# Performance work log

Hardware: AMD Instinct MI355X
Metric: run time of the kernel (lower is better)

The kernel has to match this reference:

```python
import jax, jax.numpy as jnp
import numpy as np

N = 50000      # nodes
E = 800000     # edges (avg degree 16)
F = 128        # num_features
H = 128        # hidden_channels
C = 16         # num_classes
KEEP = 0.5     # dropout keep prob


def setup_inputs() -> dict:
    key = jax.random.key(0)
    ks = jax.random.split(key, 7)
    x = jax.random.normal(ks[0], (N, F), dtype=jnp.float32)
    edge_index = jax.random.randint(ks[1], (2, E), 0, N, dtype=jnp.int64)
    W1 = jax.random.normal(ks[2], (F, H), dtype=jnp.float32) / np.float32(np.sqrt(F))
    b1 = jnp.zeros((H,), dtype=jnp.float32)
    W2 = jax.random.normal(ks[3], (H, C), dtype=jnp.float32) / np.float32(np.sqrt(H))
    b2 = jnp.zeros((C,), dtype=jnp.float32)
    # deterministic dropout mask (train-mode dropout, prob=0.5), pre-scaled by 1/keep
    dropout_mask = (jax.random.uniform(ks[4], (N, H)) < KEEP).astype(jnp.float32) / np.float32(KEEP)
    return {"x": x, "edge_index": edge_index, "W1": W1, "b1": b1,
            "W2": W2, "b2": b2, "dropout_mask": dropout_mask}


def _gather_mean(h, src, dst, n_nodes):
    # irregular gather (h[src]) + segment scatter-add at dst, then mean by in-degree
    agg = jax.ops.segment_sum(h[src], dst, num_segments=n_nodes)  # [N, c]
    deg = jax.ops.segment_sum(jnp.ones_like(dst, dtype=h.dtype), dst, num_segments=n_nodes)
    return agg / jnp.maximum(deg, 1.0)[:, None]


def reference(x, edge_index, W1, b1, W2, b2, dropout_mask):
    src, dst = edge_index[0], edge_index[1]
    # linmaps1: 0th->1st order broadcast; identity for singleton reference domains
    h = _gather_mean(x, src, dst, N)          # ConvolutionalLayer_1P #1: gather
    h = h @ W1 + b1                           # linear transform
    h = jax.nn.relu(h)
    h = h * dropout_mask                      # Dropout(prob=0.5)
    h = _gather_mean(h, src, dst, N)          # ConvolutionalLayer_1P #2: gather
    out = h @ W2 + b2
    # linmaps0: 1st->0th order reduce; identity for singleton domains
    return out
```

## Files before the change

kernel.cpp:

```cpp
#include <hip/hip_runtime.h>

#define NNODES 50000
#define NEDGES 800000
#define FDIM 128
#define HDIM 128
#define CDIM 16

#define NBUCK 256
#define BCAP 6144
#define NBA 391
#define NMB 782

typedef __attribute__((ext_vector_type(8))) short bf16x8;
typedef __attribute__((ext_vector_type(4))) float f32x4;

__device__ __forceinline__ ushort f32_to_bf16_rne(float f) {
  unsigned u = __float_as_uint(f);
  unsigned rounded = u + 0x7fffu + ((u >> 16) & 1u);
  return (ushort)(rounded >> 16);
}
__device__ __forceinline__ float bf_lo(unsigned u) { return __uint_as_float(u << 16); }
__device__ __forceinline__ float bf_hi(unsigned u) { return __uint_as_float(u & 0xffff0000u); }

__global__ __launch_bounds__(256) void k_binA(
    const int* __restrict__ src, const int* __restrict__ dst,
    int* __restrict__ gcur, unsigned* __restrict__ ebuf,
    const float* __restrict__ mask, unsigned* __restrict__ maskb) {
  __shared__ int cnt[NBUCK];
  __shared__ int base[NBUCK];
  int tid = threadIdx.x;
  if (blockIdx.x < NBA) {
    int e0 = blockIdx.x * 2048;
    cnt[tid] = 0;
    __syncthreads();
    int sv[8], dv[8];
    #pragma unroll
    for (int i = 0; i < 8; ++i) {
      int e = e0 + i * 256 + tid;
      if (e < NEDGES) {
        sv[i] = src[e];
        dv[i] = dst[e];
        atomicAdd(&cnt[dv[i] >> 8], 1);
      } else {
        dv[i] = -1;
      }
    }
    __syncthreads();
    base[tid] = atomicAdd(&gcur[tid], cnt[tid]);
    cnt[tid] = 0;
    __syncthreads();
    #pragma unroll
    for (int i = 0; i < 8; ++i) {
      if (dv[i] >= 0) {
        int b = dv[i] >> 8;
        int pos = base[b] + atomicAdd(&cnt[b], 1);
        if (pos < BCAP)
          ebuf[b * BCAP + pos] = ((unsigned)(dv[i] & 255) << 16) | (unsigned)sv[i];
      }
    }
    return;
  }
  int t = (blockIdx.x - NBA) * 256 + tid;
  if (t < 200000) {
    const float* mp = mask + (size_t)t * 32;
    unsigned bits = 0;
    #pragma unroll
    for (int i = 0; i < 8; ++i) {
      float4 m = *reinterpret_cast<const float4*>(mp + i * 4);
      bits |= (m.x != 0.f ? 1u : 0u) << (i * 4 + 0);
      bits |= (m.y != 0.f ? 1u : 0u) << (i * 4 + 1);
      bits |= (m.z != 0.f ? 1u : 0u) << (i * 4 + 2);
      bits |= (m.w != 0.f ? 1u : 0u) << (i * 4 + 3);
    }
    maskb[t] = bits;
  }
}

__global__ __launch_bounds__(256) void k_binB_cast(
    const int* __restrict__ gcur, const unsigned* __restrict__ ebuf,
    int* __restrict__ deg, int* __restrict__ offs, ushort* __restrict__ ssrc,
    const float* __restrict__ x, ushort* __restrict__ xh,
    const float* __restrict__ W1, ushort* __restrict__ W1T,
    const float* __restrict__ W2, ushort* __restrict__ W2T) {
  __shared__ int s[NBUCK];
  __shared__ int doff[NBUCK];
  __shared__ int dcur[NBUCK];
  int tid = threadIdx.x;
  if (blockIdx.x < NBUCK) {
    int b = blockIdx.x;
    int c = gcur[tid];
    if (c > BCAP) c = BCAP;
    s[tid] = c;
    for (int off = 1; off < 256; off <<= 1) {
      __syncthreads();
      int t = (tid >= off) ? s[tid - off] : 0;
      __syncthreads();
      s[tid] += t;
    }
    __syncthreads();
    int my_base = (b > 0) ? s[b - 1] : 0;
    int count = s[b] - my_base;

    dcur[tid] = 0;
    __syncthreads();
    const unsigned* eb = &ebuf[b * BCAP];
    for (int e = tid; e < count; e += 256) {
      atomicAdd(&dcur[eb[e] >> 16], 1);
    }
    __syncthreads();
    int dn = dcur[tid];
    s[tid] = dn;
    for (int off = 1; off < 256; off <<= 1) {
      __syncthreads();
      int t = (tid >= off) ? s[tid - off] : 0;
      __syncthreads();
      s[tid] += t;
    }
    __syncthreads();
    doff[tid] = s[tid] - dn;
    int node = b * 256 + tid;
    if (node < NNODES) {
      deg[node] = dn;
      offs[node] = my_base + doff[tid];
    }
    dcur[tid] = 0;
    __syncthreads();

    for (int e = tid; e < count; e += 256) {
      unsigned v = eb[e];
      int loc = v >> 16;
      int pos = my_base + doff[loc] + atomicAdd(&dcur[loc], 1);
      ssrc[pos] = (ushort)(v & 0xffffu);
    }
    return;
  }
  int t = (blockIdx.x - NBUCK) * 256 + tid;
  if (t < 1600000) {
    float4 v = *reinterpret_cast<const float4*>(&x[t * 4]);
    ushort4 o;
    o.x = f32_to_bf16_rne(v.x);
    o.y = f32_to_bf16_rne(v.y);
    o.z = f32_to_bf16_rne(v.z);
    o.w = f32_to_bf16_rne(v.w);
    *reinterpret_cast<ushort4*>(&xh[t * 4]) = o;
    return;
  }
  t -= 1600000;
  if (t < 16384) {
    int c = t >> 7, k = t & 127;
    W1T[c * 128 + k] = f32_to_bf16_rne(W1[k * 128 + c]);
    return;
  }
  t -= 16384;
  if (t < 2048) {
    int c = t >> 7, k = t & 127;
    W2T[c * 128 + k] = f32_to_bf16_rne(W2[k * 16 + c]);
  }
}

#define ACCA(A, U) do { \
    A[0] += bf_lo(U.x); A[1] += bf_hi(U.x); \
    A[2] += bf_lo(U.y); A[3] += bf_hi(U.y); \
    A[4] += bf_lo(U.z); A[5] += bf_hi(U.z); \
    A[6] += bf_lo(U.w); A[7] += bf_hi(U.w); } while (0)

#define HT_STRIDE 132
__global__ __launch_bounds__(256) void k_fused1(
    const ushort* __restrict__ xh, const int* __restrict__ offs,
    const int* __restrict__ deg, const ushort* __restrict__ ssrc,
    const ushort* __restrict__ W1T, const float* __restrict__ b1,
    const unsigned* __restrict__ maskb, const ushort* __restrict__ W2T,
    ushort* __restrict__ zh) {
  __shared__ ushort sh[16 * HT_STRIDE];
  __shared__ ushort ht[16 * HT_STRIDE];
  int tid = threadIdx.x;
  int grp = tid >> 4;
  int l16 = tid & 15;
  int nw = blockIdx.x * 16;
  int n = nw + grp;
  int start = offs[n];
  int d = deg[n];
  const ushort* base = xh + l16 * 8;
  float a0[8] = {0,0,0,0,0,0,0,0};
  float a1[8] = {0,0,0,0,0,0,0,0};
  float a2[8] = {0,0,0,0,0,0,0,0};
  float a3[8] = {0,0,0,0,0,0,0,0};
  int j = 0;
  for (; j + 7 < d; j += 8) {
    int s0 = ssrc[start + j + 0];
    int s1 = ssrc[start + j + 1];
    int s2 = ssrc[start + j + 2];
    int s3 = ssrc[start + j + 3];
    int s4 = ssrc[start + j + 4];
    int s5 = ssrc[start + j + 5];
    int s6 = ssrc[start + j + 6];
    int s7 = ssrc[start + j + 7];
    uint4 u0 = *reinterpret_cast<const uint4*>(base + s0 * FDIM);
    uint4 u1 = *reinterpret_cast<const uint4*>(base + s1 * FDIM);
    uint4 u2 = *reinterpret_cast<const uint4*>(base + s2 * FDIM);
    uint4 u3 = *reinterpret_cast<const uint4*>(base + s3 * FDIM);
    uint4 u4 = *reinterpret_cast<const uint4*>(base + s4 * FDIM);
    uint4 u5 = *reinterpret_cast<const uint4*>(base + s5 * FDIM);
    uint4 u6 = *reinterpret_cast<const uint4*>(base + s6 * FDIM);
    uint4 u7 = *reinterpret_cast<const uint4*>(base + s7 * FDIM);
    ACCA(a0, u0); ACCA(a1, u1); ACCA(a2, u2); ACCA(a3, u3);
    ACCA(a0, u4); ACCA(a1, u5); ACCA(a2, u6); ACCA(a3, u7);
  }
  for (; j + 3 < d; j += 4) {
    int s0 = ssrc[start + j + 0];
    int s1 = ssrc[start + j + 1];
    int s2 = ssrc[start + j + 2];
    int s3 = ssrc[start + j + 3];
    uint4 u0 = *reinterpret_cast<const uint4*>(base + s0 * FDIM);
    uint4 u1 = *reinterpret_cast<const uint4*>(base + s1 * FDIM);
    uint4 u2 = *reinterpret_cast<const uint4*>(base + s2 * FDIM);
    uint4 u3 = *reinterpret_cast<const uint4*>(base + s3 * FDIM);
    ACCA(a0, u0); ACCA(a1, u1); ACCA(a2, u2); ACCA(a3, u3);
  }
  for (; j < d; ++j) {
    int s0 = ssrc[start + j];
    uint4 u0 = *reinterpret_cast<const uint4*>(base + s0 * FDIM);
    ACCA(a0, u0);
  }
  float inv = 1.0f / (float)(d > 0 ? d : 1);
  unsigned r[4];
  #pragma unroll
  for (int k = 0; k < 4; ++k) {
    float e0 = (a0[2 * k] + a1[2 * k] + a2[2 * k] + a3[2 * k]) * inv;
    float e1 = (a0[2 * k + 1] + a1[2 * k + 1] + a2[2 * k + 1] + a3[2 * k + 1]) * inv;
    r[k] = (unsigned)f32_to_bf16_rne(e0) | ((unsigned)f32_to_bf16_rne(e1) << 16);
  }
  *reinterpret_cast<uint4*>(&sh[grp * HT_STRIDE + l16 * 8]) =
      (uint4){r[0], r[1], r[2], r[3]};
  __syncthreads();

  int w = tid >> 6;
  int lane = tid & 63;
  int m = lane & 15, quad = lane >> 4;
  int ct0 = 2 * w, ct1 = 2 * w + 1;

  bf16x8 af[4];
  #pragma unroll
  for (int kk = 0; kk < 4; ++kk) {
    const ushort* ap = &sh[m * HT_STRIDE + kk * 32 + quad * 8];
    ushort4 alo = *reinterpret_cast<const ushort4*>(ap);
    ushort4 ahi = *reinterpret_cast<const ushort4*>(ap + 4);
    af[kk] = (bf16x8){(short)alo.x, (short)alo.y, (short)alo.z, (short)alo.w,
                      (short)ahi.x, (short)ahi.y, (short)ahi.z, (short)ahi.w};
  }
  f32x4 acc0 = (f32x4){0.f, 0.f, 0.f, 0.f};
  f32x4 acc1 = (f32x4){0.f, 0.f, 0.f, 0.f};
  const ushort* bp0 = &W1T[(size_t)(ct0 * 16 + m) * 128 + quad * 8];
  const ushort* bp1 = &W1T[(size_t)(ct1 * 16 + m) * 128 + quad * 8];
  #pragma unroll
  for (int kk = 0; kk < 4; ++kk) {
    acc0 = __builtin_amdgcn_mfma_f32_16x16x32_bf16(
        af[kk], *reinterpret_cast<const bf16x8*>(bp0 + kk * 32), acc0, 0, 0, 0);
    acc1 = __builtin_amdgcn_mfma_f32_16x16x32_bf16(
        af[kk], *reinterpret_cast<const bf16x8*>(bp1 + kk * 32), acc1, 0, 0, 0);
  }

  unsigned mbw[4];
  #pragma unroll
  for (int rr = 0; rr < 4; ++rr) {
    mbw[rr] = maskb[(size_t)(nw + quad * 4 + rr) * 4 + w];
  }
  float bb0 = b1[ct0 * 16 + m];
  float bb1 = b1[ct1 * 16 + m];
  int sh0 = m;
  int sh1 = 16 + m;
  #pragma unroll
  for (int rr = 0; rr < 4; ++rr) {
    float v0 = acc0[rr] + bb0;
    v0 = v0 > 0.f ? v0 : 0.f;
    v0 = ((mbw[rr] >> sh0) & 1u) ? (v0 + v0) : 0.f;
    ht[(quad * 4 + rr) * HT_STRIDE + ct0 * 16 + m] = f32_to_bf16_rne(v0);
    float v1 = acc1[rr] + bb1;
    v1 = v1 > 0.f ? v1 : 0.f;
    v1 = ((mbw[rr] >> sh1) & 1u) ? (v1 + v1) : 0.f;
    ht[(quad * 4 + rr) * HT_STRIDE + ct1 * 16 + m] = f32_to_bf16_rne(v1);
  }
  __syncthreads();

  if (w == 0) {
    f32x4 zacc = (f32x4){0.f, 0.f, 0.f, 0.f};
    #pragma unroll
    for (int kk = 0; kk < 4; ++kk) {
      const ushort* ap = &ht[m * HT_STRIDE + kk * 32 + quad * 8];
      ushort4 alo = *reinterpret_cast<const ushort4*>(ap);
      ushort4 ahi = *reinterpret_cast<const ushort4*>(ap + 4);
      bf16x8 afr = (bf16x8){(short)alo.x, (short)alo.y, (short)alo.z, (short)alo.w,
                            (short)ahi.x, (short)ahi.y, (short)ahi.z, (short)ahi.w};
      bf16x8 b2f = *reinterpret_cast<const bf16x8*>(&W2T[m * 128 + kk * 32 + quad * 8]);
      zacc = __builtin_amdgcn_mfma_f32_16x16x32_bf16(afr, b2f, zacc, 0, 0, 0);
    }
    #pragma unroll
    for (int rr = 0; rr < 4; ++rr) {
      zh[(size_t)(nw + quad * 4 + rr) * 16 + m] = f32_to_bf16_rne(zacc[rr]);
    }
  }
}

__global__ __launch_bounds__(256) void k_spmm2(
    const ushort* __restrict__ zh, const int* __restrict__ offs,
    const int* __restrict__ deg, const ushort* __restrict__ ssrc,
    const float* __restrict__ b2, float* __restrict__ out) {
  int tid = threadIdx.x;
  int nl = tid >> 3, c2 = tid & 7;
  int n = blockIdx.x * 32 + nl;
  if (n >= NNODES) return;
  int start = offs[n], d = deg[n];
  const ushort* zb = zh + c2 * 2;
  float a0 = 0.f, a1 = 0.f, b0 = 0.f, b1v = 0.f;
  float c0 = 0.f, c1 = 0.f, d0 = 0.f, d1 = 0.f;
  int j = 0;
  for (; j + 7 < d; j += 8) {
    int s0 = ssrc[start + j + 0], s1 = ssrc[start + j + 1];
    int s2 = ssrc[start + j + 2], s3 = ssrc[start + j + 3];
    int s4 = ssrc[start + j + 4], s5 = ssrc[start + j + 5];
    int s6 = ssrc[start + j + 6], s7 = ssrc[start + j + 7];
    unsigned u0 = *reinterpret_cast<const unsigned*>(zb + s0 * 16);
    unsigned u1 = *reinterpret_cast<const unsigned*>(zb + s1 * 16);
    unsigned u2 = *reinterpret_cast<const unsigned*>(zb + s2 * 16);
    unsigned u3 = *reinterpret_cast<const unsigned*>(zb + s3 * 16);
    unsigned u4 = *reinterpret_cast<const unsigned*>(zb + s4 * 16);
    unsigned u5 = *reinterpret_cast<const unsigned*>(zb + s5 * 16);
    unsigned u6 = *reinterpret_cast<const unsigned*>(zb + s6 * 16);
    unsigned u7 = *reinterpret_cast<const unsigned*>(zb + s7 * 16);
    a0 += bf_lo(u0); a1 += bf_hi(u0);
    b0 += bf_lo(u1); b1v += bf_hi(u1);
    c0 += bf_lo(u2); c1 += bf_hi(u2);
    d0 += bf_lo(u3); d1 += bf_hi(u3);
    a0 += bf_lo(u4); a1 += bf_hi(u4);
    b0 += bf_lo(u5); b1v += bf_hi(u5);
    c0 += bf_lo(u6); c1 += bf_hi(u6);
    d0 += bf_lo(u7); d1 += bf_hi(u7);
  }
  for (; j < d; ++j) {
    int s0 = ssrc[start + j];
    unsigned u0 = *reinterpret_cast<const unsigned*>(zb + s0 * 16);
    a0 += bf_lo(u0); a1 += bf_hi(u0);
  }
  float inv = 1.0f / (float)(d > 0 ? d : 1);
  float o0 = ((a0 + b0) + (c0 + d0)) * inv + b2[c2 * 2 + 0];
  float o1 = ((a1 + b1v) + (c1 + d1)) * inv + b2[c2 * 2 + 1];
  float2 o; o.x = o0; o.y = o1;
  *reinterpret_cast<float2*>(&out[(size_t)n * 16 + c2 * 2]) = o;
}


extern "C" void kernel_launch(void* const* d_in, const int* in_sizes, int n_in,
                              void* d_out, int out_size, void* d_ws, size_t ws_size,
                              hipStream_t stream) {
  const float* x    = (const float*)d_in[0];
  const int*   ei   = (const int*)d_in[1];
  const float* W1   = (const float*)d_in[2];
  const float* b1   = (const float*)d_in[3];
  const float* W2   = (const float*)d_in[4];
  const float* b2   = (const float*)d_in[5];
  const float* mask = (const float*)d_in[6];
  float* out = (float*)d_out;

  const int* src = ei;
  const int* dst = ei + NEDGES;

  char* ws = (char*)d_ws;
  size_t o = 0;
  auto alloc = [&](size_t bytes) -> void* {
    void* p = ws + o;
    o += (bytes + 255) & ~(size_t)255;
    return p;
  };
  ushort*   xh    = (ushort*)alloc((size_t)NNODES * 128 * 2);
  ushort*   zh    = (ushort*)alloc((size_t)NNODES * 16 * 2);
  ushort*   W1T   = (ushort*)alloc((size_t)128 * 128 * 2);
  ushort*   W2T   = (ushort*)alloc((size_t)16 * 128 * 2);
  int*      deg   = (int*)alloc((size_t)NNODES * 4);
  int*      offs  = (int*)alloc((size_t)NNODES * 4);
  int*      gcur  = (int*)alloc((size_t)NBUCK * 4);
  unsigned* ebuf  = (unsigned*)alloc((size_t)NBUCK * BCAP * 4);
  ushort*   ssrc  = (ushort*)alloc((size_t)NEDGES * 2);
  unsigned* maskb = (unsigned*)alloc((size_t)NNODES * 4 * 4);

  int cast_blocks = (1600000 + 16384 + 2048 + 255) / 256;

  hipMemsetAsync(gcur, 0, NBUCK * sizeof(int), stream);
  k_binA<<<NBA + NMB, 256, 0, stream>>>(src, dst, gcur, ebuf, mask, maskb);
  k_binB_cast<<<NBUCK + cast_blocks, 256, 0, stream>>>(gcur, ebuf, deg, offs, ssrc,
                                                       x, xh, W1, W1T, W2, W2T);
  k_fused1<<<NNODES / 16, 256, 0, stream>>>(xh, offs, deg, ssrc,
                                            W1T, b1, maskb, W2T, zh);
  k_spmm2<<<(NNODES + 31) / 32, 256, 0, stream>>>(zh, offs, deg, ssrc, b2, out);
}
```

Before: 173.5 us.

## Merge four-kernel pipeline into one persistent cooperative kernel with grid syncs

Result: slower. 624.8 us (+260.2%).

```diff
diff --git a/kernel.cpp b/kernel.cpp
--- a/kernel.cpp
+++ b/kernel.cpp
@@ -1,15 +1,21 @@
 #include <hip/hip_runtime.h>
+#include <hip/hip_cooperative_groups.h>
+
+namespace cg = cooperative_groups;
 
 #define NNODES 50000
 #define NEDGES 800000
 #define FDIM 128
-#define HDIM 128
-#define CDIM 16
 
 #define NBUCK 256
 #define BCAP 6144
 #define NBA 391
 #define NMB 782
+#define CASTU 6322
+#define A_UNITS (NBA + NMB + CASTU)
+#define C_TILES 3125
+#define D_UNITS 1563
+#define HT_STRIDE 132
 
 typedef __attribute__((ext_vector_type(8))) short bf16x8;
 typedef __attribute__((ext_vector_type(4))) float f32x4;
@@ -22,72 +28,113 @@
 __device__ __forceinline__ float bf_lo(unsigned u) { return __uint_as_float(u << 16); }
 __device__ __forceinline__ float bf_hi(unsigned u) { return __uint_as_float(u & 0xffff0000u); }
 
-__global__ __launch_bounds__(256) void k_binA(
+#define ACCA(A, U) do { \
+    A[0] += bf_lo(U.x); A[1] += bf_hi(U.x); \
+    A[2] += bf_lo(U.y); A[3] += bf_hi(U.y); \
+    A[4] += bf_lo(U.z); A[5] += bf_hi(U.z); \
+    A[6] += bf_lo(U.w); A[7] += bf_hi(U.w); } while (0)
+
+__global__ __launch_bounds__(256, 8) void k_mega(
     const int* __restrict__ src, const int* __restrict__ dst,
-    int* __restrict__ gcur, unsigned* __restrict__ ebuf,
-    const float* __restrict__ mask, unsigned* __restrict__ maskb) {
-  __shared__ int cnt[NBUCK];
-  __shared__ int base[NBUCK];
+    const float* __restrict__ x, const float* __restrict__ W1,
+    const float* __restrict__ b1, const float* __restrict__ W2,
+    const float* __restrict__ b2, const float* __restrict__ mask,
+    float* __restrict__ out,
+    ushort* __restrict__ xh, ushort* __restrict__ zh,
+    ushort* __restrict__ W1T, ushort* __restrict__ W2T,
+    int* __restrict__ deg, int* __restrict__ offs, int* __restrict__ gcur,
+    unsigned* __restrict__ ebuf, ushort* __restrict__ ssrc,
+    unsigned* __restrict__ maskb) {
+  cg::grid_group grid = cg::this_grid();
+  __shared__ __align__(16) char smem[8448];
+  int* si = (int*)smem;
+  ushort* su = (ushort*)smem;
   int tid = threadIdx.x;
-  if (blockIdx.x < NBA) {
-    int e0 = blockIdx.x * 2048;
-    cnt[tid] = 0;
-    __syncthreads();
-    int sv[8], dv[8];
-    #pragma unroll
-    for (int i = 0; i < 8; ++i) {
-      int e = e0 + i * 256 + tid;
-      if (e < NEDGES) {
-        sv[i] = src[e];
-        dv[i] = dst[e];
-        atomicAdd(&cnt[dv[i] >> 8], 1);
+  int G = gridDim.x;
+
+  if (blockIdx.x == 0) gcur[tid] = 0;
+  grid.sync();
+
+  for (int u = blockIdx.x; u < A_UNITS; u += G) {
+    if (u < NBA) {
+      int* cnt = si;
+      int* base = si + NBUCK;
+      int e0 = u * 2048;
+      cnt[tid] = 0;
+      __syncthreads();
+      int sv[8], dv[8];
+      #pragma unroll
+      for (int i = 0; i < 8; ++i) {
+        int e = e0 + i * 256 + tid;
+        if (e < NEDGES) {
+          sv[i] = src[e];
+          dv[i] = dst[e];
+          atomicAdd(&cnt[dv[i] >> 8], 1);
+        } else {
+          dv[i] = -1;
+        }
+      }
+      __syncthreads();
+      base[tid] = atomicAdd(&gcur[tid], cnt[tid]);
+      cnt[tid] = 0;
+      __syncthreads();
+      #pragma unroll
+      for (int i = 0; i < 8; ++i) {
+        if (dv[i] >= 0) {
+          int b = dv[i] >> 8;
+          int pos = base[b] + atomicAdd(&cnt[b], 1);
+          if (pos < BCAP)
+            ebuf[b * BCAP + pos] = ((unsigned)(dv[i] & 255) << 16) | (unsigned)sv[i];
+        }
+      }
+      __syncthreads();
+    } else if (u < NBA + NMB) {
+      int t = (u - NBA) * 256 + tid;
+      if (t < 200000) {
+        const float* mp = mask + (size_t)t * 32;
+        unsigned bits = 0;
+        #pragma unroll
+        for (int i = 0; i < 8; ++i) {
+          float4 m = *reinterpret_cast<const float4*>(mp + i * 4);
+          bits |= (m.x != 0.f ? 1u : 0u) << (i * 4 + 0);
+          bits |= (m.y != 0.f ? 1u : 0u) << (i * 4 + 1);
+          bits |= (m.z != 0.f ? 1u : 0u) << (i * 4 + 2);
+          bits |= (m.w != 0.f ? 1u : 0u) << (i * 4 + 3);
+        }
+        maskb[t] = bits;
+      }
+    } else {
+      int t = (u - NBA - NMB) * 256 + tid;
+      if (t < 1600000) {
+        float4 v = *reinterpret_cast<const float4*>(&x[t * 4]);
+        ushort4 o;
+        o.x = f32_to_bf16_rne(v.x);
+        o.y = f32_to_bf16_rne(v.y);
+        o.z = f32_to_bf16_rne(v.z);
+        o.w = f32_to_bf16_rne(v.w);
+        *reinterpret_cast<ushort4*>(&xh[t * 4]) = o;
       } else {
-        dv[i] = -1;
-      }
-    }
-    __syncthreads();
-    base[tid] = atomicAdd(&gcur[tid], cnt[tid]);
-    cnt[tid] = 0;
-    __syncthreads();
-    #pragma unroll
-    for (int i = 0; i < 8; ++i) {
-      if (dv[i] >= 0) {
-        int b = dv[i] >> 8;
-        int pos = base[b] + atomicAdd(&cnt[b], 1);
-        if (pos < BCAP)
-          ebuf[b * BCAP + pos] = ((unsigned)(dv[i] & 255) << 16) | (unsigned)sv[i];
-      }
-    }
-    return;
+        t -= 1600000;
+        if (t < 16384) {
+          int c = t >> 7, k = t & 127;
+          W1T[c * 128 + k] = f32_to_bf16_rne(W1[k * 128 + c]);
+        } else {
+          t -= 16384;
+          if (t < 2048) {
+            int c = t >> 7, k = t & 127;
+            W2T[c * 128 + k] = f32_to_bf16_rne(W2[k * 16 + c]);
+          }
+        }
+      }
+    }
   }
-  int t = (blockIdx.x - NBA) * 256 + tid;
-  if (t < 200000) {
-    const float* mp = mask + (size_t)t * 32;
-    unsigned bits = 0;
-    #pragma unroll
-    for (int i = 0; i < 8; ++i) {
-      float4 m = *reinterpret_cast<const float4*>(mp + i * 4);
-      bits |= (m.x != 0.f ? 1u : 0u) << (i * 4 + 0);
-      bits |= (m.y != 0.f ? 1u : 0u) << (i * 4 + 1);
-      bits |= (m.z != 0.f ? 1u : 0u) << (i * 4 + 2);
-      bits |= (m.w != 0.f ? 1u : 0u) << (i * 4 + 3);
-    }
-    maskb[t] = bits;
-  }
-}
-
-__global__ __launch_bounds__(256) void k_binB_cast(
-    const int* __restrict__ gcur, const unsigned* __restrict__ ebuf,
-    int* __restrict__ deg, int* __restrict__ offs, ushort* __restrict__ ssrc,
-    const float* __restrict__ x, ushort* __restrict__ xh,
-    const float* __restrict__ W1, ushort* __restrict__ W1T,
-    const float* __restrict__ W2, ushort* __restrict__ W2T) {
-  __shared__ int s[NBUCK];
-  __shared__ int doff[NBUCK];
-  __shared__ int dcur[NBUCK];
-  int tid = threadIdx.x;
-  if (blockIdx.x < NBUCK) {
-    int b = blockIdx.x;
+  grid.sync();
+
+  for (int u = blockIdx.x; u < NBUCK; u += G) {
+    int* s = si;
+    int* doff = si + NBUCK;
+    int* dcur = si + 2 * NBUCK;
+    int b = u;
     int c = gcur[tid];
     if (c > BCAP) c = BCAP;
     s[tid] = c;
@@ -132,220 +179,176 @@
       int pos = my_base + doff[loc] + atomicAdd(&dcur[loc], 1);
       ssrc[pos] = (ushort)(v & 0xffffu);
     }
-    return;
+    __syncthreads();
   }
-  int t = (blockIdx.x - NBUCK) * 256 + tid;
-  if (t < 1600000) {
-    float4 v = *reinterpret_cast<const float4*>(&x[t * 4]);
-    ushort4 o;
-    o.x = f32_to_bf16_rne(v.x);
-    o.y = f32_to_bf16_rne(v.y);
-    o.z = f32_to_bf16_rne(v.z);
-    o.w = f32_to_bf16_rne(v.w);
-    *reinterpret_cast<ushort4*>(&xh[t * 4]) = o;
-    return;
-  }
-  t -= 1600000;
-  if (t < 16384) {
-    int c = t >> 7, k = t & 127;
-    W1T[c * 128 + k] = f32_to_bf16_rne(W1[k * 128 + c]);
-    return;
-  }
-  t -= 16384;
-  if (t < 2048) {
-    int c = t >> 7, k = t & 127;
-    W2T[c * 128 + k] = f32_to_bf16_rne(W2[k * 16 + c]);
-  }
-}
-
-#define ACCA(A, U) do { \
-    A[0] += bf_lo(U.x); A[1] += bf_hi(U.x); \
-    A[2] += bf_lo(U.y); A[3] += bf_hi(U.y); \
-    A[4] += bf_lo(U.z); A[5] += bf_hi(U.z); \
-    A[6] += bf_lo(U.w); A[7] += bf_hi(U.w); } while (0)
-
-#define HT_STRIDE 132
-__global__ __launch_bounds__(256) void k_fused1(
-    const ushort* __restrict__ xh, const int* __restrict__ offs,
-    const int* __restrict__ deg, const ushort* __restrict__ ssrc,
-    const ushort* __restrict__ W1T, const float* __restrict__ b1,
-    const unsigned* __restrict__ maskb, const ushort* __restrict__ W2T,
-    ushort* __restrict__ zh) {
-  __shared__ ushort sh[16 * HT_STRIDE];
-  __shared__ ushort ht[16 * HT_STRIDE];
-  int tid = threadIdx.x;
-  int grp = tid >> 4;
-  int l16 = tid & 15;
-  int nw = blockIdx.x * 16;
-  int n = nw + grp;
-  int start = offs[n];
-  int d = deg[n];
-  const ushort* base = xh + l16 * 8;
-  float a0[8] = {0,0,0,0,0,0,0,0};
-  float a1[8] = {0,0,0,0,0,0,0,0};
-  float a2[8] = {0,0,0,0,0,0,0,0};
-  float a3[8] = {0,0,0,0,0,0,0,0};
-  int j = 0;
-  for (; j + 7 < d; j += 8) {
-    int s0 = ssrc[start + j + 0];
-    int s1 = ssrc[start + j + 1];
-    int s2 = ssrc[start + j + 2];
-    int s3 = ssrc[start + j + 3];
-    int s4 = ssrc[start + j + 4];
-    int s5 = ssrc[start + j + 5];
-    int s6 = ssrc[start + j + 6];
-    int s7 = ssrc[start + j + 7];
-    uint4 u0 = *reinterpret_cast<const uint4*>(base + s0 * FDIM);
-    uint4 u1 = *reinterpret_cast<const uint4*>(base + s1 * FDIM);
-    uint4 u2 = *reinterpret_cast<const uint4*>(base + s2 * FDIM);
-    uint4 u3 = *reinterpret_cast<const uint4*>(base + s3 * FDIM);
-    uint4 u4 = *reinterpret_cast<const uint4*>(base + s4 * FDIM);
-    uint4 u5 = *reinterpret_cast<const uint4*>(base + s5 * FDIM);
-    uint4 u6 = *reinterpret_cast<const uint4*>(base + s6 * FDIM);
-    uint4 u7 = *reinterpret_cast<const uint4*>(base + s7 * FDIM);
-    ACCA(a0, u0); ACCA(a1, u1); ACCA(a2, u2); ACCA(a3, u3);
-    ACCA(a0, u4); ACCA(a1, u5); ACCA(a2, u6); ACCA(a3, u7);
-  }
-  for (; j + 3 < d; j += 4) {
-    int s0 = ssrc[start + j + 0];
-    int s1 = ssrc[start + j + 1];
-    int s2 = ssrc[start + j + 2];
-    int s3 = ssrc[start + j + 3];
-    uint4 u0 = *reinterpret_cast<const uint4*>(base + s0 * FDIM);
-    uint4 u1 = *reinterpret_cast<const uint4*>(base + s1 * FDIM);
-    uint4 u2 = *reinterpret_cast<const uint4*>(base + s2 * FDIM);
-    uint4 u3 = *reinterpret_cast<const uint4*>(base + s3 * FDIM);
-    ACCA(a0, u0); ACCA(a1, u1); ACCA(a2, u2); ACCA(a3, u3);
-  }
-  for (; j < d; ++j) {
-    int s0 = ssrc[start + j];
-    uint4 u0 = *reinterpret_cast<const uint4*>(base + s0 * FDIM);
-    ACCA(a0, u0);
-  }
-  float inv = 1.0f / (float)(d > 0 ? d : 1);
-  unsigned r[4];
-  #pragma unroll
-  for (int k = 0; k < 4; ++k) {
-    float e0 = (a0[2 * k] + a1[2 * k] + a2[2 * k] + a3[2 * k]) * inv;
-    float e1 = (a0[2 * k + 1] + a1[2 * k + 1] + a2[2 * k + 1] + a3[2 * k + 1]) * inv;
-    r[k] = (unsigned)f32_to_bf16_rne(e0) | ((unsigned)f32_to_bf16_rne(e1) << 16);
-  }
-  *reinterpret_cast<uint4*>(&sh[grp * HT_STRIDE + l16 * 8]) =
-      (uint4){r[0], r[1], r[2], r[3]};
-  __syncthreads();
-
-  int w = tid >> 6;
-  int lane = tid & 63;
-  int m = lane & 15, quad = lane >> 4;
-  int ct0 = 2 * w, ct1 = 2 * w + 1;
-
-  bf16x8 af[4];
-  #pragma unroll
-  for (int kk = 0; kk < 4; ++kk) {
-    const ushort* ap = &sh[m * HT_STRIDE + kk * 32 + quad * 8];
-    ushort4 alo = *reinterpret_cast<const ushort4*>(ap);
-    ushort4 ahi = *reinterpret_cast<const ushort4*>(ap + 4);
-    af[kk] = (bf16x8){(short)alo.x, (short)alo.y, (short)alo.z, (short)alo.w,
-                      (short)ahi.x, (short)ahi.y, (short)ahi.z, (short)ahi.w};
-  }
-  f32x4 acc0 = (f32x4){0.f, 0.f, 0.f, 0.f};
-  f32x4 acc1 = (f32x4){0.f, 0.f, 0.f, 0.f};
-  const ushort* bp0 = &W1T[(size_t)(ct0 * 16 + m) * 128 + quad * 8];
-  const ushort* bp1 = &W1T[(size_t)(ct1 * 16 + m) * 128 + quad * 8];
-  #pragma unroll
-  for (int kk = 0; kk < 4; ++kk) {
-    acc0 = __builtin_amdgcn_mfma_f32_16x16x32_bf16(
-        af[kk], *reinterpret_cast<const bf16x8*>(bp0 + kk * 32), acc0, 0, 0, 0);
-    acc1 = __builtin_amdgcn_mfma_f32_16x16x32_bf16(
-        af[kk], *reinterpret_cast<const bf16x8*>(bp1 + kk * 32), acc1, 0, 0, 0);
-  }
-
-  unsigned mbw[4];
-  #pragma unroll
-  for (int rr = 0; rr < 4; ++rr) {
-    mbw[rr] = maskb[(size_t)(nw + quad * 4 + rr) * 4 + w];
-  }
-  float bb0 = b1[ct0 * 16 + m];
-  float bb1 = b1[ct1 * 16 + m];
-  int sh0 = m;
-  int sh1 = 16 + m;
-  #pragma unroll
-  for (int rr = 0; rr < 4; ++rr) {
-    float v0 = acc0[rr] + bb0;
-    v0 = v0 > 0.f ? v0 : 0.f;
-    v0 = ((mbw[rr] >> sh0) & 1u) ? (v0 + v0) : 0.f;
-    ht[(quad * 4 + rr) * HT_STRIDE + ct0 * 16 + m] = f32_to_bf16_rne(v0);
-    float v1 = acc1[rr] + bb1;
-    v1 = v1 > 0.f ? v1 : 0.f;
-    v1 = ((mbw[rr] >> sh1) & 1u) ? (v1 + v1) : 0.f;
-    ht[(quad * 4 + rr) * HT_STRIDE + ct1 * 16 + m] = f32_to_bf16_rne(v1);
-  }
-  __syncthreads();
-
-  if (w == 0) {
-    f32x4 zacc = (f32x4){0.f, 0.f, 0.f, 0.f};
+  grid.sync();
+
+  for (int u = blockIdx.x; u < C_TILES; u += G) {
+    ushort* sh = su;
+    ushort* ht = su + 2112;
+    int grp = tid >> 4;
+    int l16 = tid & 15;
+    int nw = u * 16;
+    int n = nw + grp;
+    int start = offs[n];
+    int d = deg[n];
+    const ushort* base = xh + l16 * 8;
+    float a0[8] = {0,0,0,0,0,0,0,0};
+    float a1[8] = {0,0,0,0,0,0,0,0};
+    float a2[8] = {0,0,0,0,0,0,0,0};
+    float a3[8] = {0,0,0,0,0,0,0,0};
+    int j = 0;
+    for (; j + 3 < d; j += 4) {
+      int s0 = ssrc[start + j + 0];
+      int s1 = ssrc[start + j + 1];
+      int s2 = ssrc[start + j + 2];
+      int s3 = ssrc[start + j + 3];
+      uint4 u0 = *reinterpret_cast<const uint4*>(base + s0 * FDIM);
+      uint4 u1 = *reinterpret_cast<const uint4*>(base + s1 * FDIM);
+      uint4 u2 = *reinterpret_cast<const uint4*>(base + s2 * FDIM);
+      uint4 u3 = *reinterpret_cast<const uint4*>(base + s3 * FDIM);
+      ACCA(a0, u0); ACCA(a1, u1); ACCA(a2, u2); ACCA(a3, u3);
+    }
+    if (j < d) {
+      int s0 = ssrc[start + j];
+      uint4 u0 = *reinterpret_cast<const uint4*>(base + s0 * FDIM);
+      ACCA(a0, u0);
+      ++j;
+      if (j < d) {
+        int s1 = ssrc[start + j];
+        uint4 u1 = *reinterpret_cast<const uint4*>(base + s1 * FDIM);
+        ACCA(a1, u1);
+        ++j;
+        if (j < d) {
+          int s2 = ssrc[start + j];
+          uint4 u2 = *reinterpret_cast<const uint4*>(base + s2 * FDIM);
+          ACCA(a2, u2);
+        }
+      }
+    }
+    float inv = 1.0f / (float)(d > 0 ? d : 1);
+    unsigned r[4];
+    #pragma unroll
+    for (int k = 0; k < 4; ++k) {
+      float e0 = (a0[2 * k] + a1[2 * k] + a2[2 * k] + a3[2 * k]) * inv;
+      float e1 = (a0[2 * k + 1] + a1[2 * k + 1] + a2[2 * k + 1] + a3[2 * k + 1]) * inv;
+      r[k] = (unsigned)f32_to_bf16_rne(e0) | ((unsigned)f32_to_bf16_rne(e1) << 16);
+    }
+    *reinterpret_cast<uint4*>(&sh[grp * HT_STRIDE + l16 * 8]) =
+        (uint4){r[0], r[1], r[2], r[3]};
+    __syncthreads();
+
+    int w = tid >> 6;
+    int lane = tid & 63;
+    int m = lane & 15, quad = lane >> 4;
+    int ct0 = 2 * w, ct1 = 2 * w + 1;
+
+    bf16x8 af[4];
     #pragma unroll
     for (int kk = 0; kk < 4; ++kk) {
-      const ushort* ap = &ht[m * HT_STRIDE + kk * 32 + quad * 8];
+      const ushort* ap = &sh[m * HT_STRIDE + kk * 32 + quad * 8];
       ushort4 alo = *reinterpret_cast<const ushort4*>(ap);
       ushort4 ahi = *reinterpret_cast<const ushort4*>(ap + 4);
-      bf16x8 afr = (bf16x8){(short)alo.x, (short)alo.y, (short)alo.z, (short)alo.w,
-                            (short)ahi.x, (short)ahi.y, (short)ahi.z, (short)ahi.w};
-      bf16x8 b2f = *reinterpret_cast<const bf16x8*>(&W2T[m * 128 + kk * 32 + quad * 8]);
-      zacc = __builtin_amdgcn_mfma_f32_16x16x32_bf16(afr, b2f, zacc, 0, 0, 0);
-    }
+      af[kk] = (bf16x8){(short)alo.x, (short)alo.y, (short)alo.z, (short)alo.w,
+                        (short)ahi.x, (short)ahi.y, (short)ahi.z, (short)ahi.w};
+    }
+    f32x4 acc0 = (f32x4){0.f, 0.f, 0.f, 0.f};
+    f32x4 acc1 = (f32x4){0.f, 0.f, 0.f, 0.f};
+    const ushort* bp0 = &W1T[(size_t)(ct0 * 16 + m) * 128 + quad * 8];
+    const ushort* bp1 = &W1T[(size_t)(ct1 * 16 + m) * 128 + quad * 8];
+    #pragma unroll
+    for (int kk = 0; kk < 4; ++kk) {
+      acc0 = __builtin_amdgcn_mfma_f32_16x16x32_bf16(
+          af[kk], *reinterpret_cast<const bf16x8*>(bp0 + kk * 32), acc0, 0, 0, 0);
+      acc1 = __builtin_amdgcn_mfma_f32_16x16x32_bf16(
+          af[kk], *reinterpret_cast<const bf16x8*>(bp1 + kk * 32), acc1, 0, 0, 0);
+    }
+
+    unsigned mbw[4];
     #pragma unroll
     for (int rr = 0; rr < 4; ++rr) {
-      zh[(size_t)(nw + quad * 4 + rr) * 16 + m] = f32_to_bf16_rne(zacc[rr]);
+      mbw[rr] = maskb[(size_t)(nw + quad * 4 + rr) * 4 + w];
+    }
+    float bb0 = b1[ct0 * 16 + m];
+    float bb1 = b1[ct1 * 16 + m];
+    int sh0 = m;
+    int sh1 = 16 + m;
+    #pragma unroll
+    for (int rr = 0; rr < 4; ++rr) {
+      float v0 = acc0[rr] + bb0;
+      v0 = v0 > 0.f ? v0 : 0.f;
+      v0 = ((mbw[rr] >> sh0) & 1u) ? (v0 + v0) : 0.f;
+      ht[(quad * 4 + rr) * HT_STRIDE + ct0 * 16 + m] = f32_to_bf16_rne(v0);
+      float v1 = acc1[rr] + bb1;
+      v1 = v1 > 0.f ? v1 : 0.f;
+      v1 = ((mbw[rr] >> sh1) & 1u) ? (v1 + v1) : 0.f;
+      ht[(quad * 4 + rr) * HT_STRIDE + ct1 * 16 + m] = f32_to_bf16_rne(v1);
+    }
+    __syncthreads();
+
+    if (w == 0) {
+      f32x4 zacc = (f32x4){0.f, 0.f, 0.f, 0.f};
+      #pragma unroll
+      for (int kk = 0; kk < 4; ++kk) {
+        const ushort* ap = &ht[m * HT_STRIDE + kk * 32 + quad * 8];
+        ushort4 alo = *reinterpret_cast<const ushort4*>(ap);
+        ushort4 ahi = *reinterpret_cast<const ushort4*>(ap + 4);
+        bf16x8 afr = (bf16x8){(short)alo.x, (short)alo.y, (short)alo.z, (short)alo.w,
+                              (short)ahi.x, (short)ahi.y, (short)ahi.z, (short)ahi.w};
+        bf16x8 b2f = *reinterpret_cast<const bf16x8*>(&W2T[m * 128 + kk * 32 + quad * 8]);
+        zacc = __builtin_amdgcn_mfma_f32_16x16x32_bf16(afr, b2f, zacc, 0, 0, 0);
+      }
+      #pragma unroll
+      for (int rr = 0; rr < 4; ++rr) {
+        zh[(size_t)(nw + quad * 4 + rr) * 16 + m] = f32_to_bf16_rne(zacc[rr]);
+      }
     }
   }
-}
-
-__global__ __launch_bounds__(256) void k_spmm2(
-    const ushort* __restrict__ zh, const int* __restrict__ offs,
-    const int* __restrict__ deg, const ushort* __restrict__ ssrc,
-    const float* __restrict__ b2, float* __restrict__ out) {
-  int tid = threadIdx.x;
-  int nl = tid >> 3, c2 = tid & 7;
-  int n = blockIdx.x * 32 + nl;
-  if (n >= NNODES) return;
-  int start = offs[n], d = deg[n];
-  const ushort* zb = zh + c2 * 2;
-  float a0 = 0.f, a1 = 0.f, b0 = 0.f, b1v = 0.f;
-  float c0 = 0.f, c1 = 0.f, d0 = 0.f, d1 = 0.f;
-  int j = 0;
-  for (; j + 7 < d; j += 8) {
-    int s0 = ssrc[start + j + 0], s1 = ssrc[start + j + 1];
-    int s2 = ssrc[start + j + 2], s3 = ssrc[start + j + 3];
-    int s4 = ssrc[start + j + 4], s5 = ssrc[start + j + 5];
-    int s6 = ssrc[start + j + 6], s7 = ssrc[start + j + 7];
-    unsigned u0 = *reinterpret_cast<const unsigned*>(zb + s0 * 16);
-    unsigned u1 = *reinterpret_cast<const unsigned*>(zb + s1 * 16);
-    unsigned u2 = *reinterpret_cast<const unsigned*>(zb + s2 * 16);
-    unsigned u3 = *reinterpret_cast<const unsigned*>(zb + s3 * 16);
-    unsigned u4 = *reinterpret_cast<const unsigned*>(zb + s4 * 16);
-    unsigned u5 = *reinterpret_cast<const unsigned*>(zb + s5 * 16);
-    unsigned u6 = *reinterpret_cast<const unsigned*>(zb + s6 * 16);
-    unsigned u7 = *reinterpret_cast<const unsigned*>(zb + s7 * 16);
-    a0 += bf_lo(u0); a1 += bf_hi(u0);
-    b0 += bf_lo(u1); b1v += bf_hi(u1);
-    c0 += bf_lo(u2); c1 += bf_hi(u2);
-    d0 += bf_lo(u3); d1 += bf_hi(u3);
-    a0 += bf_lo(u4); a1 += bf_hi(u4);
-    b0 += bf_lo(u5); b1v += bf_hi(u5);
-    c0 += bf_lo(u6); c1 += bf_hi(u6);
-    d0 += bf_lo(u7); d1 += bf_hi(u7);
+  grid.sync();
+
+  for (int u = blockIdx.x; u < D_UNITS; u += G) {
+    int nl = tid >> 3, c2 = tid & 7;
+    int n = u * 32 + nl;
+    if (n < NNODES) {
+      int start = offs[n], d = deg[n];
+      const ushort* zb = zh + c2 * 2;
+      float a0 = 0.f, a1 = 0.f, b0 = 0.f, b1v = 0.f;
+      float c0 = 0.f, c1 = 0.f, d0 = 0.f, d1 = 0.f;
+      int j = 0;
+      for (; j + 7 < d; j += 8) {
+        int s0 = ssrc[start + j + 0], s1 = ssrc[start + j + 1];
+        int s2 = ssrc[start + j + 2], s3 = ssrc[start + j + 3];
+        int s4 = ssrc[start + j + 4], s5 = ssrc[start + j + 5];
+        int s6 = ssrc[start + j + 6], s7 = ssrc[start + j + 7];
+        unsigned u0 = *reinterpret_cast<const unsigned*>(zb + s0 * 16);
+        unsigned u1 = *reinterpret_cast<const unsigned*>(zb + s1 * 16);
+        unsigned u2 = *reinterpret_cast<const unsigned*>(zb + s2 * 16);
+        unsigned u3 = *reinterpret_cast<const unsigned*>(zb + s3 * 16);
+        unsigned u4 = *reinterpret_cast<const unsigned*>(zb + s4 * 16);
+        unsigned u5 = *reinterpret_cast<const unsigned*>(zb + s5 * 16);
+        unsigned u6 = *reinterpret_cast<const unsigned*>(zb + s6 * 16);
+        unsigned u7 = *reinterpret_cast<const unsigned*>(zb + s7 * 16);
+        a0 += bf_lo(u0); a1 += bf_hi(u0);
+        b0 += bf_lo(u1); b1v += bf_hi(u1);
+        c0 += bf_lo(u2); c1 += bf_hi(u2);
+        d0 += bf_lo(u3); d1 += bf_hi(u3);
+        a0 += bf_lo(u4); a1 += bf_hi(u4);
+        b0 += bf_lo(u5); b1v += bf_hi(u5);
+        c0 += bf_lo(u6); c1 += bf_hi(u6);
+        d0 += bf_lo(u7); d1 += bf_hi(u7);
+      }
+      for (; j < d; ++j) {
+        int s0 = ssrc[start + j];
+        unsigned u0 = *reinterpret_cast<const unsigned*>(zb + s0 * 16);
+        a0 += bf_lo(u0); a1 += bf_hi(u0);
+      }
+      float inv = 1.0f / (float)(d > 0 ? d : 1);
+      float o0 = ((a0 + b0) + (c0 + d0)) * inv + b2[c2 * 2 + 0];
+      float o1 = ((a1 + b1v) + (c1 + d1)) * inv + b2[c2 * 2 + 1];
+      float2 o; o.x = o0; o.y = o1;
+      *reinterpret_cast<float2*>(&out[(size_t)n * 16 + c2 * 2]) = o;
+    }
   }
-  for (; j < d; ++j) {
-    int s0 = ssrc[start + j];
-    unsigned u0 = *reinterpret_cast<const unsigned*>(zb + s0 * 16);
-    a0 += bf_lo(u0); a1 += bf_hi(u0);
-  }
-  float inv = 1.0f / (float)(d > 0 ? d : 1);
-  float o0 = ((a0 + b0) + (c0 + d0)) * inv + b2[c2 * 2 + 0];
-  float o1 = ((a1 + b1v) + (c1 + d1)) * inv + b2[c2 * 2 + 1];
-  float2 o; o.x = o0; o.y = o1;
-  *reinterpret_cast<float2*>(&out[(size_t)n * 16 + c2 * 2]) = o;
 }
 
 
@@ -382,13 +385,18 @@
   ushort*   ssrc  = (ushort*)alloc((size_t)NEDGES * 2);
   unsigned* maskb = (unsigned*)alloc((size_t)NNODES * 4 * 4);
 
-  int cast_blocks = (1600000 + 16384 + 2048 + 255) / 256;
-
-  hipMemsetAsync(gcur, 0, NBUCK * sizeof(int), stream);
-  k_binA<<<NBA + NMB, 256, 0, stream>>>(src, dst, gcur, ebuf, mask, maskb);
-  k_binB_cast<<<NBUCK + cast_blocks, 256, 0, stream>>>(gcur, ebuf, deg, offs, ssrc,
-                                                       x, xh, W1, W1T, W2, W2T);
-  k_fused1<<<NNODES / 16, 256, 0, stream>>>(xh, offs, deg, ssrc,
-                                            W1T, b1, maskb, W2T, zh);
-  k_spmm2<<<(NNODES + 31) / 32, 256, 0, stream>>>(zh, offs, deg, ssrc, b2, out);
+  int blocksPerCU = 0;
+  (void)hipOccupancyMaxActiveBlocksPerMultiprocessor(&blocksPerCU, k_mega, 256, 0);
+  int nblk = blocksPerCU * 256;
+  if (nblk > 2048) nblk = 2048;
+  if (nblk < 256) nblk = 256;
+
+  void* args[] = {
+      (void*)&src, (void*)&dst, (void*)&x, (void*)&W1, (void*)&b1,
+      (void*)&W2, (void*)&b2, (void*)&mask, (void*)&out,
+      (void*)&xh, (void*)&zh, (void*)&W1T, (void*)&W2T,
+      (void*)&deg, (void*)&offs, (void*)&gcur, (void*)&ebuf,
+      (void*)&ssrc, (void*)&maskb};
+  (void)hipLaunchCooperativeKernel((void*)k_mega, dim3(nblk), dim3(256),
+                                   args, 0, stream);
 }
```
